# Kernel tuning notes

Measured on AMD Instinct MI355X. Metric: run time of the kernel, lower is better.

## Reference

```python
import jax, jax.numpy as jnp
import numpy as np
from jax import lax

NUM_WORDS, WORD_DIM = 50000, 300
NUM_CHARS, CHAR_DIM = 100, 100
NUM_POS, POS_DIM = 50, 100
NUM_FILTERS, KERNEL = 100, 3
PRIVACY_TERMS = (3, 7, 11)


def setup_inputs() -> dict:
    key = jax.random.key(0)
    ks = jax.random.split(key, 8)
    bs, ls, cl = 64, 512, 32
    return {
        "input_word": jax.random.randint(ks[0], (bs, ls), 0, NUM_WORDS, dtype=jnp.int64 if jax.config.jax_enable_x64 else jnp.int32),
        "input_char": jax.random.randint(ks[1], (bs, ls, cl), 0, NUM_CHARS),
        "input_pos": jax.random.randint(ks[2], (bs, ls), 0, NUM_POS),
        "word_table": jax.random.normal(ks[3], (NUM_WORDS, WORD_DIM), jnp.float32) * 0.1,
        "char_table": jax.random.normal(ks[4], (NUM_CHARS, CHAR_DIM), jnp.float32) * 0.1,
        "pos_table": jax.random.normal(ks[5], (NUM_POS, POS_DIM), jnp.float32) * 0.1,
        "conv_w": jax.random.normal(ks[6], (NUM_FILTERS, CHAR_DIM, KERNEL), jnp.float32) * 0.05,
        "conv_b": jax.random.normal(ks[7], (NUM_FILTERS,), jnp.float32) * 0.05,
    }


def _dist_feature(input_pos):
    # nearest-privacy-token distance: parallel prefix-min via cummax/cummin scans
    priv = jnp.asarray(PRIVACY_TERMS)
    pri_mask = (input_pos[..., None] == priv).any(-1)           # [bs, ls]
    ls = input_pos.shape[1]
    pos_idx = jnp.arange(ls)                                      # [ls]
    last = lax.cummax(jnp.where(pri_mask, pos_idx, -1000), axis=1)                 # last privacy idx <= j
    nxt = lax.cummin(jnp.where(pri_mask, pos_idx, 1000), axis=1, reverse=True)     # next privacy idx >= j
    dis = jnp.minimum(pos_idx - last, nxt - pos_idx).astype(jnp.float32)
    return dis[..., None]                                         # [bs, ls, 1]


def _char_cnn(char_emb, conv_w, conv_b):
    # char_emb: [bs, ls, cl, char_dim] -> [bs, ls, num_filters]
    bs, ls, cl, cd = char_emb.shape
    x = char_emb.reshape(bs * ls, cl, cd).transpose(0, 2, 1)      # [N, C, L]
    y = lax.conv_general_dilated(x, conv_w, window_strides=(1,),
                                 padding=[(KERNEL - 1, KERNEL - 1)],
                                 dimension_numbers=("NCH", "OIH", "NCH"))
    y = y + conv_b[None, :, None]
    y = jnp.tanh(y.max(axis=2))                                   # max over length, then tanh
    return y.reshape(bs, ls, -1)


def reference(input_word, input_char, input_pos, word_table, char_table, pos_table, conv_w, conv_b):
    dis = _dist_feature(input_pos)
    word = word_table[input_word]                                 # [bs, ls, word_dim]
    char = _char_cnn(char_table[input_char], conv_w, conv_b)      # [bs, ls, num_filters]
    pos = pos_table[input_pos]                                    # [bs, ls, pos_dim]
    return jnp.concatenate([dis, word, char, pos], axis=2)
```

## Files before the change

kernel.cpp:

```cpp
#include <hip/hip_runtime.h>
#include <hip/hip_fp16.h>

#define BS 64
#define LS 512
#define CL 32
#define WD 300
#define NC 100
#define CD 100
#define PD 100
#define NF 100
#define KK 3
#define OPAD 128
#define PROW (KK*OPAD)
#define PBYTES (NC*PROW*2)
#define NV4 (PBYTES/16)
#define OUTD 501
#define TPB 64
#define NTHR 1024

typedef _Float16 h2 __attribute__((ext_vector_type(2)));

__global__ void precompute_P(const float* __restrict__ conv_w,
                             const float* __restrict__ char_table,
                             _Float16* __restrict__ P) {
    const int c = blockIdx.x;
    const int k = blockIdx.y;
    const int o = threadIdx.x;
    __shared__ float row[CD];
    if (o < CD) row[o] = char_table[c * CD + o];
    __syncthreads();
    float acc = 0.f;
    if (o < NF) {
        const float* w = conv_w + o * (CD * KK) + k;
        #pragma unroll 4
        for (int i = 0; i < CD; ++i) acc += w[i * KK] * row[i];
    }
    P[(c * KK + k) * OPAD + o] = (_Float16)acc;
}

__global__ __launch_bounds__(NTHR, 8) void main_kernel(
        const int* __restrict__ input_word,
        const int* __restrict__ input_char,
        const int* __restrict__ input_pos,
        const float* __restrict__ word_table,
        const float* __restrict__ pos_table,
        const float* __restrict__ conv_b,
        const _Float16* __restrict__ Pg,
        float* __restrict__ out) {
    __shared__ alignas(16) _Float16 Pl[NC * PROW];
    __shared__ alignas(16) unsigned char s_char[TPB * CL];
    __shared__ unsigned long long s_mask[LS / 64];

    const int tid  = threadIdx.x;
    const int tok0 = blockIdx.x * TPB;

    const uint4* src = (const uint4*)Pg;
    const uint4 s0 = src[tid];
    const uint4 s1 = src[tid + NTHR];
    const uint4 s2 = src[tid + 2 * NTHR];
    const uint4 s3 = src[tid + 3 * NTHR];
    uint4 s4 = {};
    const bool h4 = (tid + 4 * NTHR) < NV4;
    if (h4) s4 = src[tid + 4 * NTHR];

    const int row = tok0 >> 9;
    if (tid < LS) {
        const int p = input_pos[row * LS + tid];
        const bool pm = (p == 3) | (p == 7) | (p == 11);
        const unsigned long long b = __ballot(pm);
        if ((tid & 63) == 0) s_mask[tid >> 6] = b;
    }

    if (tid < (TPB * CL) / 4) {
        const int4 c4 = ((const int4*)(input_char + tok0 * CL))[tid];
        ((unsigned*)s_char)[tid] =
            (unsigned)c4.x | ((unsigned)c4.y << 8) | ((unsigned)c4.z << 16) | ((unsigned)c4.w << 24);
    }

    for (int i = tid; i < TPB * (WD / 4); i += NTHR) {
        const int t = i / (WD / 4);
        const int j = i - t * (WD / 4);
        const int w = input_word[tok0 + t];
        const float4 v = ((const float4*)word_table)[(size_t)w * (WD / 4) + j];
        float* o = out + (size_t)(tok0 + t) * OUTD + 1 + 4 * j;
        o[0] = v.x; o[1] = v.y; o[2] = v.z; o[3] = v.w;
    }

    {
        uint4* dst = (uint4*)Pl;
        dst[tid] = s0;
        dst[tid + NTHR] = s1;
        dst[tid + 2 * NTHR] = s2;
        dst[tid + 3 * NTHR] = s3;
        if (h4) dst[tid + 4 * NTHR] = s4;
    }
    __syncthreads();

    const int tl = tid >> 4;
    const int l  = tid & 15;
    const unsigned* s_cw = (const unsigned*)s_char;
    const char* Pb = (const char*)Pl + l * 16;
    h2 a0[4], a1[4], m[4];
    #pragma unroll
    for (int i = 0; i < 4; ++i) {
        a0[i] = (h2)(_Float16)0;
        a1[i] = (h2)(_Float16)0;
        m[i]  = (h2)(_Float16)(-60000.f);
    }
    #pragma unroll 2
    for (int w = 0; w < CL / 4; ++w) {
        const unsigned wd = s_cw[tl * (CL / 4) + w];
        #pragma unroll
        for (int b = 0; b < 4; ++b) {
            const int ca = (int)((wd >> (8 * b)) & 0xFFu) * (PROW * 2);
            const uint4 r0 = *(const uint4*)(Pb + ca + 0 * (OPAD * 2));
            const uint4 r1 = *(const uint4*)(Pb + ca + 1 * (OPAD * 2));
            const uint4 r2 = *(const uint4*)(Pb + ca + 2 * (OPAD * 2));
            #pragma unroll
            for (int i = 0; i < 4; ++i) {
                const unsigned c0 = (i == 0) ? r0.x : (i == 1) ? r0.y : (i == 2) ? r0.z : r0.w;
                const unsigned c1 = (i == 0) ? r1.x : (i == 1) ? r1.y : (i == 2) ? r1.z : r1.w;
                const unsigned c2 = (i == 0) ? r2.x : (i == 1) ? r2.y : (i == 2) ? r2.z : r2.w;
                const h2 p0 = __builtin_bit_cast(h2, c0);
                const h2 p1 = __builtin_bit_cast(h2, c1);
                const h2 p2 = __builtin_bit_cast(h2, c2);
                const h2 y = a0[i] + p2;
                m[i]  = __builtin_elementwise_max(m[i], y);
                a0[i] = a1[i] + p1;
                a1[i] = p0;
            }
        }
    }
    if (l < 13) {
        float mm[8];
        #pragma unroll
        for (int i = 0; i < 4; ++i) {
            const h2 v = __builtin_elementwise_max(m[i], __builtin_elementwise_max(a0[i], a1[i]));
            mm[2 * i]     = (float)v.x;
            mm[2 * i + 1] = (float)v.y;
        }
        const float4 b0 = *(const float4*)(conv_b + 8 * l);
        float* outc = out + (size_t)(tok0 + tl) * OUTD + 301 + 8 * l;
        outc[0] = tanhf(mm[0] + b0.x);
        outc[1] = tanhf(mm[1] + b0.y);
        outc[2] = tanhf(mm[2] + b0.z);
        outc[3] = tanhf(mm[3] + b0.w);
        if (l < 12) {
            const float4 b1 = *(const float4*)(conv_b + 8 * l + 4);
            outc[4] = tanhf(mm[4] + b1.x);
            outc[5] = tanhf(mm[5] + b1.y);
            outc[6] = tanhf(mm[6] + b1.z);
            outc[7] = tanhf(mm[7] + b1.w);
        }
    }

    for (int i = tid; i < TPB * (PD / 4); i += NTHR) {
        const int t = i / (PD / 4);
        const int j = i - t * (PD / 4);
        const int p = input_pos[tok0 + t];
        const float4 v = ((const float4*)pos_table)[p * (PD / 4) + j];
        float* o = out + (size_t)(tok0 + t) * OUTD + 401 + 4 * j;
        o[0] = v.x; o[1] = v.y; o[2] = v.z; o[3] = v.w;
    }

    if (tid < TPB) {
        const int j = (tok0 & (LS - 1)) + tid;
        const int wj = j >> 6, bj = j & 63;
        int last = -1000;
        {
            unsigned long long x = s_mask[wj] & ((2ull << bj) - 1ull);
            int w = wj;
            while (true) {
                if (x) { last = w * 64 + 63 - __clzll(x); break; }
                if (--w < 0) break;
                x = s_mask[w];
            }
        }
        int nxt = 1000;
        {
            unsigned long long x = s_mask[wj] & (~0ull << bj);
            int w = wj;
            while (true) {
                if (x) { nxt = w * 64 + (int)__ffsll((long long)x) - 1; break; }
                if (++w >= LS / 64) break;
                x = s_mask[w];
            }
        }
        out[(size_t)(tok0 + tid) * OUTD] = (float)min(j - last, nxt - j);
    }
}

extern "C" void kernel_launch(void* const* d_in, const int* in_sizes, int n_in,
                              void* d_out, int out_size, void* d_ws, size_t ws_size,
                              hipStream_t stream) {
    const int*   input_word = (const int*)d_in[0];
    const int*   input_char = (const int*)d_in[1];
    const int*   input_pos  = (const int*)d_in[2];
    const float* word_table = (const float*)d_in[3];
    const float* char_table = (const float*)d_in[4];
    const float* pos_table  = (const float*)d_in[5];
    const float* conv_w     = (const float*)d_in[6];
    const float* conv_b     = (const float*)d_in[7];
    float* out = (float*)d_out;

    _Float16* P = (_Float16*)d_ws;

    precompute_P<<<dim3(NC, KK), 128, 0, stream>>>(conv_w, char_table, P);
    main_kernel<<<(BS * LS) / TPB, NTHR, 0, stream>>>(
        input_word, input_char, input_pos, word_table, pos_table, conv_b, P, out);
}
```

Baseline: 42.63 us.

## Warp-specialize block: half computes char CNN, half streams word/pos gathers

Splits the 1024-thread block into two halves. The first 512 threads run the char-CNN loop over two passes of 32 tokens each. The other 512 threads copy the word and pos embeddings and compute the distance feature. Before, the word gather ran before the barrier and the CNN was serialized behind it; now the memory-bound copies overlap with the LDS-bound convolution inside each block. The trade-off is that each half has half the threads for its work, so the CNN takes twice as many iterations per thread.

```diff
diff --git a/kernel.cpp b/kernel.cpp
--- a/kernel.cpp
+++ b/kernel.cpp
@@ -60,12 +60,11 @@
     const uint4 s2 = src[tid + 2 * NTHR];
     const uint4 s3 = src[tid + 3 * NTHR];
     uint4 s4 = {};
-    const bool h4 = (tid + 4 * NTHR) < NV4;
+    const bool h4 = tid < (NV4 - 4 * NTHR);
     if (h4) s4 = src[tid + 4 * NTHR];
 
-    const int row = tok0 >> 9;
     if (tid < LS) {
-        const int p = input_pos[row * LS + tid];
+        const int p = input_pos[(tok0 >> 9) * LS + tid];
         const bool pm = (p == 3) | (p == 7) | (p == 11);
         const unsigned long long b = __ballot(pm);
         if ((tid & 63) == 0) s_mask[tid >> 6] = b;
@@ -75,15 +74,6 @@
         const int4 c4 = ((const int4*)(input_char + tok0 * CL))[tid];
         ((unsigned*)s_char)[tid] =
             (unsigned)c4.x | ((unsigned)c4.y << 8) | ((unsigned)c4.z << 16) | ((unsigned)c4.w << 24);
-    }
-
-    for (int i = tid; i < TPB * (WD / 4); i += NTHR) {
-        const int t = i / (WD / 4);
-        const int j = i - t * (WD / 4);
-        const int w = input_word[tok0 + t];
-        const float4 v = ((const float4*)word_table)[(size_t)w * (WD / 4) + j];
-        float* o = out + (size_t)(tok0 + t) * OUTD + 1 + 4 * j;
-        o[0] = v.x; o[1] = v.y; o[2] = v.z; o[3] = v.w;
     }
 
     {
@@ -96,97 +86,114 @@
     }
     __syncthreads();
 
-    const int tl = tid >> 4;
-    const int l  = tid & 15;
-    const unsigned* s_cw = (const unsigned*)s_char;
-    const char* Pb = (const char*)Pl + l * 16;
-    h2 a0[4], a1[4], m[4];
-    #pragma unroll
-    for (int i = 0; i < 4; ++i) {
-        a0[i] = (h2)(_Float16)0;
-        a1[i] = (h2)(_Float16)0;
-        m[i]  = (h2)(_Float16)(-60000.f);
-    }
-    #pragma unroll 2
-    for (int w = 0; w < CL / 4; ++w) {
-        const unsigned wd = s_cw[tl * (CL / 4) + w];
-        #pragma unroll
-        for (int b = 0; b < 4; ++b) {
-            const int ca = (int)((wd >> (8 * b)) & 0xFFu) * (PROW * 2);
-            const uint4 r0 = *(const uint4*)(Pb + ca + 0 * (OPAD * 2));
-            const uint4 r1 = *(const uint4*)(Pb + ca + 1 * (OPAD * 2));
-            const uint4 r2 = *(const uint4*)(Pb + ca + 2 * (OPAD * 2));
+    if (tid < 512) {
+        const int wid  = tid >> 6;
+        const int lane = tid & 63;
+        const int l    = lane & 15;
+        const char* Pb = (const char*)Pl + l * 16;
+        const unsigned* s_cw = (const unsigned*)s_char;
+
+        #pragma unroll 1
+        for (int pass = 0; pass < 2; ++pass) {
+            const int tb = wid * 8 + pass * 4 + (lane >> 4);
+            h2 a0[4], a1[4], m[4];
             #pragma unroll
             for (int i = 0; i < 4; ++i) {
-                const unsigned c0 = (i == 0) ? r0.x : (i == 1) ? r0.y : (i == 2) ? r0.z : r0.w;
-                const unsigned c1 = (i == 0) ? r1.x : (i == 1) ? r1.y : (i == 2) ? r1.z : r1.w;
-                const unsigned c2 = (i == 0) ? r2.x : (i == 1) ? r2.y : (i == 2) ? r2.z : r2.w;
-                const h2 p0 = __builtin_bit_cast(h2, c0);
-                const h2 p1 = __builtin_bit_cast(h2, c1);
-                const h2 p2 = __builtin_bit_cast(h2, c2);
-                const h2 y = a0[i] + p2;
-                m[i]  = __builtin_elementwise_max(m[i], y);
-                a0[i] = a1[i] + p1;
-                a1[i] = p0;
-            }
-        }
-    }
-    if (l < 13) {
-        float mm[8];
-        #pragma unroll
-        for (int i = 0; i < 4; ++i) {
-            const h2 v = __builtin_elementwise_max(m[i], __builtin_elementwise_max(a0[i], a1[i]));
-            mm[2 * i]     = (float)v.x;
-            mm[2 * i + 1] = (float)v.y;
-        }
-        const float4 b0 = *(const float4*)(conv_b + 8 * l);
-        float* outc = out + (size_t)(tok0 + tl) * OUTD + 301 + 8 * l;
-        outc[0] = tanhf(mm[0] + b0.x);
-        outc[1] = tanhf(mm[1] + b0.y);
-        outc[2] = tanhf(mm[2] + b0.z);
-        outc[3] = tanhf(mm[3] + b0.w);
-        if (l < 12) {
-            const float4 b1 = *(const float4*)(conv_b + 8 * l + 4);
-            outc[4] = tanhf(mm[4] + b1.x);
-            outc[5] = tanhf(mm[5] + b1.y);
-            outc[6] = tanhf(mm[6] + b1.z);
-            outc[7] = tanhf(mm[7] + b1.w);
-        }
-    }
-
-    for (int i = tid; i < TPB * (PD / 4); i += NTHR) {
-        const int t = i / (PD / 4);
-        const int j = i - t * (PD / 4);
-        const int p = input_pos[tok0 + t];
-        const float4 v = ((const float4*)pos_table)[p * (PD / 4) + j];
-        float* o = out + (size_t)(tok0 + t) * OUTD + 401 + 4 * j;
-        o[0] = v.x; o[1] = v.y; o[2] = v.z; o[3] = v.w;
-    }
-
-    if (tid < TPB) {
-        const int j = (tok0 & (LS - 1)) + tid;
-        const int wj = j >> 6, bj = j & 63;
-        int last = -1000;
-        {
-            unsigned long long x = s_mask[wj] & ((2ull << bj) - 1ull);
-            int w = wj;
-            while (true) {
-                if (x) { last = w * 64 + 63 - __clzll(x); break; }
-                if (--w < 0) break;
-                x = s_mask[w];
-            }
-        }
-        int nxt = 1000;
-        {
-            unsigned long long x = s_mask[wj] & (~0ull << bj);
-            int w = wj;
-            while (true) {
-                if (x) { nxt = w * 64 + (int)__ffsll((long long)x) - 1; break; }
-                if (++w >= LS / 64) break;
-                x = s_mask[w];
-            }
-        }
-        out[(size_t)(tok0 + tid) * OUTD] = (float)min(j - last, nxt - j);
+                a0[i] = (h2)(_Float16)0;
+                a1[i] = (h2)(_Float16)0;
+                m[i]  = (h2)(_Float16)(-60000.f);
+            }
+            #pragma unroll 2
+            for (int w = 0; w < CL / 4; ++w) {
+                const unsigned wd = s_cw[tb * (CL / 4) + w];
+                #pragma unroll
+                for (int b = 0; b < 4; ++b) {
+                    const int ca = (int)((wd >> (8 * b)) & 0xFFu) * (PROW * 2);
+                    const uint4 r0 = *(const uint4*)(Pb + ca + 0 * (OPAD * 2));
+                    const uint4 r1 = *(const uint4*)(Pb + ca + 1 * (OPAD * 2));
+                    const uint4 r2 = *(const uint4*)(Pb + ca + 2 * (OPAD * 2));
+                    #pragma unroll
+                    for (int i = 0; i < 4; ++i) {
+                        const unsigned c0 = (i == 0) ? r0.x : (i == 1) ? r0.y : (i == 2) ? r0.z : r0.w;
+                        const unsigned c1 = (i == 0) ? r1.x : (i == 1) ? r1.y : (i == 2) ? r1.z : r1.w;
+                        const unsigned c2 = (i == 0) ? r2.x : (i == 1) ? r2.y : (i == 2) ? r2.z : r2.w;
+                        const h2 p0 = __builtin_bit_cast(h2, c0);
+                        const h2 p1 = __builtin_bit_cast(h2, c1);
+                        const h2 p2 = __builtin_bit_cast(h2, c2);
+                        const h2 y = a0[i] + p2;
+                        m[i]  = __builtin_elementwise_max(m[i], y);
+                        a0[i] = a1[i] + p1;
+                        a1[i] = p0;
+                    }
+                }
+            }
+            if (l < 13) {
+                float mm[8];
+                #pragma unroll
+                for (int i = 0; i < 4; ++i) {
+                    const h2 v = __builtin_elementwise_max(m[i], __builtin_elementwise_max(a0[i], a1[i]));
+                    mm[2 * i]     = (float)v.x;
+                    mm[2 * i + 1] = (float)v.y;
+                }
+                const float4 b0 = *(const float4*)(conv_b + 8 * l);
+                float* outc = out + (size_t)(tok0 + tb) * OUTD + 301 + 8 * l;
+                outc[0] = tanhf(mm[0] + b0.x);
+                outc[1] = tanhf(mm[1] + b0.y);
+                outc[2] = tanhf(mm[2] + b0.z);
+                outc[3] = tanhf(mm[3] + b0.w);
+                if (l < 12) {
+                    const float4 b1 = *(const float4*)(conv_b + 8 * l + 4);
+                    outc[4] = tanhf(mm[4] + b1.x);
+                    outc[5] = tanhf(mm[5] + b1.y);
+                    outc[6] = tanhf(mm[6] + b1.z);
+                    outc[7] = tanhf(mm[7] + b1.w);
+                }
+            }
+        }
+    } else {
+        const int t2 = tid - 512;
+
+        for (int i = t2; i < TPB * (WD / 4); i += 512) {
+            const int t = i / (WD / 4);
+            const int j = i - t * (WD / 4);
+            const int w = input_word[tok0 + t];
+            const float4 v = ((const float4*)word_table)[(size_t)w * (WD / 4) + j];
+            float* o = out + (size_t)(tok0 + t) * OUTD + 1 + 4 * j;
+            o[0] = v.x; o[1] = v.y; o[2] = v.z; o[3] = v.w;
+        }
+        for (int i = t2; i < TPB * (PD / 4); i += 512) {
+            const int t = i / (PD / 4);
+            const int j = i - t * (PD / 4);
+            const int p = input_pos[tok0 + t];
+            const float4 v = ((const float4*)pos_table)[p * (PD / 4) + j];
+            float* o = out + (size_t)(tok0 + t) * OUTD + 401 + 4 * j;
+            o[0] = v.x; o[1] = v.y; o[2] = v.z; o[3] = v.w;
+        }
+        if (t2 < TPB) {
+            const int j = (tok0 & (LS - 1)) + t2;
+            const int wj = j >> 6, bj = j & 63;
+            int last = -1000;
+            {
+                unsigned long long x = s_mask[wj] & ((2ull << bj) - 1ull);
+                int w = wj;
+                while (true) {
+                    if (x) { last = w * 64 + 63 - __clzll(x); break; }
+                    if (--w < 0) break;
+                    x = s_mask[w];
+                }
+            }
+            int nxt = 1000;
+            {
+                unsigned long long x = s_mask[wj] & (~0ull << bj);
+                int w = wj;
+                while (true) {
+                    if (x) { nxt = w * 64 + (int)__ffsll((long long)x) - 1; break; }
+                    if (++w >= LS / 64) break;
+                    x = s_mask[w];
+                }
+            }
+            out[(size_t)(tok0 + t2) * OUTD] = (float)min(j - last, nxt - j);
+        }
     }
 }
 
```

Result: faster. 38.90 us (-8.7%).
